# Performance work log

Measured on AMD Instinct MI355X. Metric: run time of the kernel, lower is better.

Reference implementation:

```python
import jax, jax.numpy as jnp
import numpy as np

EPS = 1e-8  # torch F.cosine_similarity eps
TEMP = 2.0  # hardcoded in module regardless of init arg


def _normalize(x):
    # row-normalize with torch-style eps clamp on the norm
    norm = jnp.sqrt(jnp.sum(x * x, axis=-1, keepdims=True))
    return x / jnp.maximum(norm, EPS)


def setup_inputs() -> dict:
    key = jax.random.key(0)
    k1, k2, k3 = jax.random.split(key, 3)
    n, m, d = 8192, 8192, 256
    return {
        "pos_key": jax.random.normal(k1, (n, d), dtype=jnp.float32),
        "pos_value": jax.random.normal(k2, (n, d), dtype=jnp.float32),
        "neg_value": jax.random.normal(k3, (m, d), dtype=jnp.float32),
    }


def reference(pos_key, pos_value, neg_value):
    pk = _normalize(pos_key)    # [n, d]
    pv = _normalize(pos_value)  # [n, d]
    nv = _normalize(neg_value)  # [m, d]

    pos_sim = jnp.sum(pk * pv, axis=-1)          # [n]
    neg_sim = jnp.einsum("nd,md->nm", pk, nv)    # [n, m] cosine sims

    pos_loss = -jnp.mean(pos_sim / TEMP)
    # log-sum-exp over m (stable), matching log(sum(exp(.)))
    neg_loss = jnp.mean(jax.scipy.special.logsumexp(neg_sim / TEMP, axis=-1))
    return pos_loss + neg_loss
```

## Files before the change

kernel.cpp:

```cpp
#include <hip/hip_runtime.h>

typedef __attribute__((ext_vector_type(4))) float f32x4;
typedef __attribute__((ext_vector_type(4))) int   i32x4;
typedef __attribute__((ext_vector_type(8))) int   i32x8;

#define DIM 256
#define D4  64

#define GLD_LDS16(g, l) __builtin_amdgcn_global_load_lds(                      \
    (const __attribute__((address_space(1))) void*)(g),                        \
    (__attribute__((address_space(3))) void*)(l), 16, 0, 0)

__global__ __launch_bounds__(256) void normalize_kernel(
    const float4* __restrict__ pk, const float4* __restrict__ pv,
    const float4* __restrict__ nv, unsigned int* __restrict__ pkn,
    unsigned int* __restrict__ nvn, float* __restrict__ posPart, int N) {
  int row  = blockIdx.x * 4 + (threadIdx.x >> 6);
  int lane = threadIdx.x & 63;
  if (row < N) {
    float4 x = pk[row * D4 + lane];
    float4 y = pv[row * D4 + lane];
    float skk = x.x*x.x + x.y*x.y + x.z*x.z + x.w*x.w;
    float svv = y.x*y.x + y.y*y.y + y.z*y.z + y.w*y.w;
    float skv = x.x*y.x + x.y*y.y + x.z*y.z + x.w*y.w;
#pragma unroll
    for (int m = 32; m >= 1; m >>= 1) {
      skk += __shfl_xor(skk, m, 64);
      svv += __shfl_xor(svv, m, 64);
      skv += __shfl_xor(skv, m, 64);
    }
    float nk  = fmaxf(sqrtf(skk), 1e-8f);
    float nvv = fmaxf(sqrtf(svv), 1e-8f);
    if (lane == 0) posPart[row] = skv / (nk * nvv);
    float rk = 1.0f / nk;
    int w = __builtin_amdgcn_cvt_pk_fp8_f32(x.x * rk, x.y * rk, 0, false);
    w = __builtin_amdgcn_cvt_pk_fp8_f32(x.z * rk, x.w * rk, w, true);
    pkn[(size_t)row * 64 + lane] = (unsigned int)w;
  } else {
    int r2 = row - N;
    float4 x = nv[r2 * D4 + lane];
    float s = x.x*x.x + x.y*x.y + x.z*x.z + x.w*x.w;
#pragma unroll
    for (int m = 32; m >= 1; m >>= 1) s += __shfl_xor(s, m, 64);
    float rn = 1.0f / fmaxf(sqrtf(s), 1e-8f);
    int w = __builtin_amdgcn_cvt_pk_fp8_f32(x.x * rn, x.y * rn, 0, false);
    w = __builtin_amdgcn_cvt_pk_fp8_f32(x.z * rn, x.w * rn, w, true);
    nvn[(size_t)r2 * 64 + lane] = (unsigned int)w;
  }
}

__global__ __launch_bounds__(256, 3) void gemm_lse_kernel(
    const unsigned char* __restrict__ gA, const unsigned char* __restrict__ gB,
    float* __restrict__ partial, int N) {
  __shared__ unsigned char As[16384];
  __shared__ unsigned char Bs[16384];

  const int tid  = threadIdx.x;
  const int lane = tid & 63;
  const int wv   = tid >> 6;
  const int wm   = wv >> 1, wn = wv & 1;
  const int l15  = lane & 15, q = lane >> 4;
  const int row0 = blockIdx.y * 128;
  const int col0 = blockIdx.x * 128;
  const float kLog2eHalf = 0.72134752044448170f;
  const int kUnitScale = 0x7F7F7F7F;

  f32x4 acc[4][4];
#pragma unroll
  for (int mi = 0; mi < 4; mi++)
#pragma unroll
    for (int ni = 0; ni < 4; ni++) acc[mi][ni] = (f32x4){0.f, 0.f, 0.f, 0.f};

#pragma unroll
  for (int kb = 0; kb < 2; kb++) {
    if (kb) __syncthreads();
#pragma unroll
    for (int i = 0; i < 4; i++) {
      int c  = i * 256 + tid;
      int r  = c >> 3;
      int sc = ((c & 7) ^ (r & 7)) << 4;
      GLD_LDS16(gA + (size_t)(row0 + r) * 256 + kb * 128 + sc, As + c * 16);
      GLD_LDS16(gB + (size_t)(col0 + r) * 256 + kb * 128 + sc, Bs + c * 16);
    }
    __syncthreads();

    i32x8 bf[4];
#pragma unroll
    for (int ni = 0; ni < 4; ni++) {
      int r  = wn * 64 + ni * 16 + l15;
      int c0 = (q * 2)     ^ (r & 7);
      int c1 = (q * 2 + 1) ^ (r & 7);
      i32x4 lo = *(const i32x4*)(Bs + r * 128 + c0 * 16);
      i32x4 hi = *(const i32x4*)(Bs + r * 128 + c1 * 16);
      bf[ni] = (i32x8){lo.x, lo.y, lo.z, lo.w, hi.x, hi.y, hi.z, hi.w};
    }
#pragma unroll
    for (int mi = 0; mi < 4; mi++) {
      int r  = wm * 64 + mi * 16 + l15;
      int c0 = (q * 2)     ^ (r & 7);
      int c1 = (q * 2 + 1) ^ (r & 7);
      i32x4 lo = *(const i32x4*)(As + r * 128 + c0 * 16);
      i32x4 hi = *(const i32x4*)(As + r * 128 + c1 * 16);
      i32x8 af = (i32x8){lo.x, lo.y, lo.z, lo.w, hi.x, hi.y, hi.z, hi.w};
#pragma unroll
      for (int ni = 0; ni < 4; ni++)
        acc[mi][ni] = __builtin_amdgcn_mfma_scale_f32_16x16x128_f8f6f4(
            af, bf[ni], acc[mi][ni],
            0, 0, 0, kUnitScale, 0, kUnitScale);
    }
  }

  float keep = 0.f;
#pragma unroll
  for (int mi = 0; mi < 4; mi++)
#pragma unroll
    for (int rr = 0; rr < 4; rr++) {
      float v = 0.f;
#pragma unroll
      for (int ni = 0; ni < 4; ni++)
        v += __builtin_amdgcn_exp2f(acc[mi][ni][rr] * kLog2eHalf);
      v += __shfl_xor(v, 1, 16);
      v += __shfl_xor(v, 2, 16);
      v += __shfl_xor(v, 4, 16);
      v += __shfl_xor(v, 8, 16);
      if (l15 == mi * 4 + rr) keep = v;
    }
  int lrow = (l15 >> 2) * 16 + q * 4 + (l15 & 3);
  partial[(size_t)(blockIdx.x * 2 + wn) * N + row0 + wm * 64 + lrow] = keep;
}

__global__ __launch_bounds__(256) void finalize_kernel(
    const float* __restrict__ partial, const float* __restrict__ posPart,
    float* __restrict__ out, int N, int slabsPerGroup, float invN) {
  __shared__ float red[4][64];
  int t  = threadIdx.x;
  int rl = t & 63, g = t >> 6;
  int row = blockIdx.x * 64 + rl;
  const float* p = partial + (size_t)(g * slabsPerGroup) * N + row;
  float s = 0.f;
#pragma unroll 8
  for (int j = 0; j < slabsPerGroup; j++) s += p[(size_t)j * N];
  red[g][rl] = s;
  __syncthreads();
  if (t < 64) {
    float tot = red[0][rl] + red[1][rl] + red[2][rl] + red[3][rl];
    float v = __builtin_amdgcn_logf(tot) * 0.69314718055994531f
              - 0.5f * posPart[row];
#pragma unroll
    for (int m = 32; m >= 1; m >>= 1) v += __shfl_xor(v, m, 64);
    if (rl == 0) atomicAdd(out, v * invN);
  }
}

extern "C" void kernel_launch(void* const* d_in, const int* in_sizes, int n_in,
                              void* d_out, int out_size, void* d_ws, size_t ws_size,
                              hipStream_t stream) {
  const float* pk = (const float*)d_in[0];
  const float* pv = (const float*)d_in[1];
  const float* nv = (const float*)d_in[2];
  int N = in_sizes[0] / DIM;
  int M = in_sizes[2] / DIM;
  float* out = (float*)d_out;

  unsigned char* pkn = (unsigned char*)d_ws;
  unsigned char* nvn = pkn + (size_t)N * DIM;
  float* partial = (float*)(nvn + (size_t)M * DIM);
  float* posPart = partial + (size_t)(M / 64) * N;

  hipMemsetAsync(out, 0, sizeof(float), stream);

  normalize_kernel<<<(N + M) / 4, 256, 0, stream>>>(
      (const float4*)pk, (const float4*)pv, (const float4*)nv,
      (unsigned int*)pkn, (unsigned int*)nvn, posPart, N);

  gemm_lse_kernel<<<dim3(M / 128, N / 128), 256, 0, stream>>>(
      pkn, nvn, partial, N);

  finalize_kernel<<<N / 64, 256, 0, stream>>>(
      partial, posPart, out, N, (M / 64) / 4, 1.0f / (float)N);
}
```

Baseline: 107.4 us.

## Load GEMM fragments directly from global memory instead of staging through LDS

The GEMM+LSE kernel no longer copies A/B tiles into shared memory with global_load_lds and swizzled reads. Each wave instead loads its MFMA operand fragments straight from global memory (32-byte vector loads per lane), which removes the LDS traffic and both __syncthreads barriers. Because each wave pair shares rows, data is reread from global/L2 rather than reused through LDS, and the per-lane loads are strided by row, which may hurt coalescing. It also raises register pressure, since all eight fragments are held at once.

```diff
diff --git a/kernel.cpp b/kernel.cpp
--- a/kernel.cpp
+++ b/kernel.cpp
@@ -6,10 +6,6 @@
 
 #define DIM 256
 #define D4  64
-
-#define GLD_LDS16(g, l) __builtin_amdgcn_global_load_lds(                      \
-    (const __attribute__((address_space(1))) void*)(g),                        \
-    (__attribute__((address_space(3))) void*)(l), 16, 0, 0)
 
 __global__ __launch_bounds__(256) void normalize_kernel(
     const float4* __restrict__ pk, const float4* __restrict__ pv,
@@ -52,9 +48,6 @@
 __global__ __launch_bounds__(256, 3) void gemm_lse_kernel(
     const unsigned char* __restrict__ gA, const unsigned char* __restrict__ gB,
     float* __restrict__ partial, int N) {
-  __shared__ unsigned char As[16384];
-  __shared__ unsigned char Bs[16384];
-
   const int tid  = threadIdx.x;
   const int lane = tid & 63;
   const int wv   = tid >> 6;
@@ -65,6 +58,9 @@
   const float kLog2eHalf = 0.72134752044448170f;
   const int kUnitScale = 0x7F7F7F7F;
 
+  const unsigned char* aB = gA + (size_t)(row0 + wm * 64 + l15) * 256 + q * 32;
+  const unsigned char* bB = gB + (size_t)(col0 + wn * 64 + l15) * 256 + q * 32;
+
   f32x4 acc[4][4];
 #pragma unroll
   for (int mi = 0; mi < 4; mi++)
@@ -73,41 +69,20 @@
 
 #pragma unroll
   for (int kb = 0; kb < 2; kb++) {
-    if (kb) __syncthreads();
+    i32x8 af[4], bf[4];
 #pragma unroll
-    for (int i = 0; i < 4; i++) {
-      int c  = i * 256 + tid;
-      int r  = c >> 3;
-      int sc = ((c & 7) ^ (r & 7)) << 4;
-      GLD_LDS16(gA + (size_t)(row0 + r) * 256 + kb * 128 + sc, As + c * 16);
-      GLD_LDS16(gB + (size_t)(col0 + r) * 256 + kb * 128 + sc, Bs + c * 16);
-    }
-    __syncthreads();
-
-    i32x8 bf[4];
+    for (int mi = 0; mi < 4; mi++)
+      af[mi] = *(const i32x8*)(aB + mi * 4096 + kb * 128);
 #pragma unroll
-    for (int ni = 0; ni < 4; ni++) {
-      int r  = wn * 64 + ni * 16 + l15;
-      int c0 = (q * 2)     ^ (r & 7);
-      int c1 = (q * 2 + 1) ^ (r & 7);
-      i32x4 lo = *(const i32x4*)(Bs + r * 128 + c0 * 16);
-      i32x4 hi = *(const i32x4*)(Bs + r * 128 + c1 * 16);
-      bf[ni] = (i32x8){lo.x, lo.y, lo.z, lo.w, hi.x, hi.y, hi.z, hi.w};
-    }
+    for (int ni = 0; ni < 4; ni++)
+      bf[ni] = *(const i32x8*)(bB + ni * 4096 + kb * 128);
 #pragma unroll
-    for (int mi = 0; mi < 4; mi++) {
-      int r  = wm * 64 + mi * 16 + l15;
-      int c0 = (q * 2)     ^ (r & 7);
-      int c1 = (q * 2 + 1) ^ (r & 7);
-      i32x4 lo = *(const i32x4*)(As + r * 128 + c0 * 16);
-      i32x4 hi = *(const i32x4*)(As + r * 128 + c1 * 16);
-      i32x8 af = (i32x8){lo.x, lo.y, lo.z, lo.w, hi.x, hi.y, hi.z, hi.w};
+    for (int mi = 0; mi < 4; mi++)
 #pragma unroll
       for (int ni = 0; ni < 4; ni++)
         acc[mi][ni] = __builtin_amdgcn_mfma_scale_f32_16x16x128_f8f6f4(
-            af, bf[ni], acc[mi][ni],
+            af[mi], bf[ni], acc[mi][ni],
             0, 0, 0, kUnitScale, 0, kUnitScale);
-    }
   }
 
   float keep = 0.f;
```

Result: slower. 136.4 us (+27.0%).
